# Kernel optimization log

Hardware: AMD Instinct MI355X
Metric: run time of the kernel (lower is better)

## Reference

```python
import jax, jax.numpy as jnp
import numpy as np

LAMBDA = 25.0
MU = 25.0
NU = 1.0
ALPHA = 0.25
EPS = 1e-4
NUM_MATCHES = (20, 4)


def _cdist(a, b):
    # a: (B, Na, D), b: (B, Nb, D) -> euclidean distances (B, Na, Nb)
    d2 = (jnp.sum(a * a, axis=-1)[:, :, None]
          + jnp.sum(b * b, axis=-1)[:, None, :]
          - 2.0 * jnp.einsum('bnd,bmd->bnm', a, b))
    return jnp.sqrt(jnp.maximum(d2, 0.0))


def _nearest_neighbors(input_maps, candidate_maps, distances, num_matches):
    # Faithful to lightly.models.utils.nearest_neighbors:
    #  1) for each input element find its nearest candidate (argmin over last dim)
    #  2) keep the num_matches input elements with smallest nn distance
    # Indices are non-differentiable in torch, so stop_gradient on distances.
    distances = jax.lax.stop_gradient(distances)
    nn_idx = jnp.argmin(distances, axis=-1)           # (B, Na)
    nn_val = jnp.min(distances, axis=-1)              # (B, Na)
    _, min_idx = jax.lax.top_k(-nn_val, num_matches)  # smallest num_matches -> (B, M)
    filt_in = jnp.take_along_axis(input_maps, min_idx[..., None], axis=1)      # (B, M, C)
    cand_nn = jnp.take_along_axis(candidate_maps, nn_idx[..., None], axis=1)   # (B, Na, C)
    filt_cand = jnp.take_along_axis(cand_nn, min_idx[..., None], axis=1)       # (B, M, C)
    return filt_in, filt_cand


def _mse(a, b):
    return jnp.mean((a - b) ** 2)


def _variance_loss(x):
    # torch.var default is unbiased (ddof=1)
    std = jnp.sqrt(jnp.var(x, axis=0, ddof=1) + EPS)
    return jnp.mean(jax.nn.relu(1.0 - std))


def _covariance_loss(x):
    n, d = x.shape
    x = x - jnp.mean(x, axis=0)
    cov = (x.T @ x) / (n - 1)                         # (D, D)
    off = cov - jnp.diag(jnp.diag(cov))
    return jnp.sum(off ** 2) / d


def _global_loss(z_a, z_b):
    inv = _mse(z_a, z_b)
    var = 0.5 * (_variance_loss(z_a) + _variance_loss(z_b))
    cov = _covariance_loss(z_a) + _covariance_loss(z_b)
    return LAMBDA * inv + MU * var + NU * cov


def _local_loss(za, zb, ga, gb):
    B = za.shape[0]
    za = za.reshape(B, -1, za.shape[-1])              # (B, H*W, C)
    zb = zb.reshape(B, -1, zb.shape[-1])
    ga = ga.reshape(B, -1, 2)                          # (B, H*W, 2)
    gb = gb.reshape(B, -1, 2)
    has_local_view = za.shape[1] != zb.shape[1]
    nm = NUM_MATCHES[1] if has_local_view else NUM_MATCHES[0]
    # L2 feature-space matching
    fa, na = _nearest_neighbors(za, zb, _cdist(za, zb), nm)
    fb, nb = _nearest_neighbors(zb, za, _cdist(zb, za), nm)
    inv = 0.5 * _mse(fa, na) + 0.5 * _mse(fb, nb)
    # Grid (spatial) matching
    fa, na = _nearest_neighbors(za, zb, _cdist(ga, gb), NUM_MATCHES[0])
    fb, nb = _nearest_neighbors(zb, za, _cdist(gb, ga), NUM_MATCHES[1])
    inv = inv + 0.5 * _mse(fa, na) + 0.5 * _mse(fb, nb)
    return LAMBDA * inv


def setup_inputs() -> dict:
    key = jax.random.key(0)
    k1, k2, k3, k4, k5, k6 = jax.random.split(key, 6)
    B, D = 128, 8192
    H = W = 7
    return {
        'z_a': jax.random.normal(k1, (B, D), dtype=jnp.float32),
        'z_b': jax.random.normal(k2, (B, D), dtype=jnp.float32),
        'z_a_local_features': jax.random.normal(k3, (B, H, W, D), dtype=jnp.float32),
        'z_b_local_features': jax.random.normal(k4, (B, H, W, D), dtype=jnp.float32),
        'grid_a': jax.random.uniform(k5, (B, H, W, 2), dtype=jnp.float32),
        'grid_b': jax.random.uniform(k6, (B, H, W, 2), dtype=jnp.float32),
    }


def reference(z_a, z_b, z_a_local_features, z_b_local_features, grid_a, grid_b):
    g = _global_loss(z_a, z_b)
    l = _local_loss(z_a_local_features, z_b_local_features, grid_a, grid_b)
    return ALPHA * g + (1.0 - ALPHA) * l
```

## Files before the change

kernel.cpp:

```cpp
#include <hip/hip_runtime.h>
#include <math.h>

#define BATCH 128
#define DIM   8192
#define HW    49
#define PAIRS 2401
#define SLOT  2512

#define WS_MSE    0
#define WS_VARA   1
#define WS_VARB   2
#define WS_DIAGA  3
#define WS_DIAGB  4
#define WS_S1     5
#define WS_S2     6
#define WS_S3     7
#define WS_S4     8
#define WS_SK2A   9
#define WS_SK2B   10
#define WS_TICKET 11
#define COLS_OFF    16
#define GRAMA_OFF   32784
#define GRAMB_OFF   49168
#define GK2PART_OFF 65552
#define L1PART_BIG  2162704
#define WS_NEED_FLOATS (L1PART_BIG + 256 * SLOT)
#define L1PART_SMALL 65552

typedef __attribute__((ext_vector_type(8))) short bf16x8;
typedef __attribute__((ext_vector_type(4))) float f32x4;

__device__ __forceinline__ unsigned cvtpk(float lo, float hi) {
    unsigned r;
    asm("v_cvt_pk_bf16_f32 %0, %1, %2" : "=v"(r) : "v"(lo), "v"(hi));
    return r;
}
__device__ __forceinline__ bf16x8 cvt8(f32x4 a, f32x4 b) {
    union { unsigned u[4]; bf16x8 v; } r;
    r.u[0] = cvtpk(a.x, a.y); r.u[1] = cvtpk(a.z, a.w);
    r.u[2] = cvtpk(b.x, b.y); r.u[3] = cvtpk(b.z, b.w);
    return r.v;
}
__device__ __forceinline__ f32x4 ld4(const unsigned char* p) {
    return *(const f32x4*)p;
}
__device__ __forceinline__ void gload16(const float* g, unsigned char* l) {
    __builtin_amdgcn_global_load_lds(
        (const __attribute__((address_space(1))) void*)g,
        (__attribute__((address_space(3))) void*)l, 16, 0, 0);
}

template<bool RED>
__global__ __launch_bounds__(512) void uber(const float* __restrict__ za_l,
                                            const float* __restrict__ zb_l,
                                            const float* __restrict__ z_a,
                                            const float* __restrict__ z_b,
                                            float* __restrict__ ws,
                                            float* __restrict__ l1part)
{
    __shared__ __align__(16) unsigned char shm[150528];
    const int tid = threadIdx.x;

    if (blockIdx.x < 64) {
        const int chunk = blockIdx.x;
        float* sxA = (float*)shm;
        float* sxB = sxA + 128 * 68;
        float* scr = sxB + 128 * 68;
        const int ty = tid >> 5, tx = tid & 31;
        const int q = tid >> 6, cc = tid & 63;

        float accA[8][4], accB[8][4];
#pragma unroll
        for (int r = 0; r < 8; ++r)
#pragma unroll
            for (int c = 0; c < 4; ++c) { accA[r][c] = 0.f; accB[r][c] = 0.f; }
        float cSA[2] = {0.f,0.f}, cQA[2] = {0.f,0.f};
        float cSB[2] = {0.f,0.f}, cQB[2] = {0.f,0.f};
        float mse = 0.f;

#pragma unroll
        for (int st = 0; st < 2; ++st) {
            __syncthreads();
            for (int f = tid; f < 2048; f += 512) {
                int row = f >> 4, c4 = f & 15;
                const float4 a4 = *(const float4*)(z_a + (size_t)row * DIM + chunk * 128 + st * 64 + c4 * 4);
                const float4 b4 = *(const float4*)(z_b + (size_t)row * DIM + chunk * 128 + st * 64 + c4 * 4);
                *(float4*)(sxA + row * 68 + c4 * 4) = a4;
                *(float4*)(sxB + row * 68 + c4 * 4) = b4;
                float dx = a4.x - b4.x, dy = a4.y - b4.y, dz = a4.z - b4.z, dw = a4.w - b4.w;
                mse += dx * dx + dy * dy + dz * dz + dw * dw;
            }
            __syncthreads();
            for (int r = 0; r < 16; ++r) {
                float vA = sxA[(q * 16 + r) * 68 + cc];
                float vB = sxB[(q * 16 + r) * 68 + cc];
                cSA[st] += vA; cQA[st] += vA * vA;
                cSB[st] += vB; cQB[st] += vB * vB;
            }
            for (int k = 0; k < 64; k += 4) {
                float4 ar4[8], br4[8];
#pragma unroll
                for (int r = 0; r < 8; ++r) {
                    ar4[r] = *(const float4*)(sxA + (ty + 16 * r) * 68 + k);
                    br4[r] = *(const float4*)(sxB + (ty + 16 * r) * 68 + k);
                }
#pragma unroll
                for (int c = 0; c < 4; ++c) {
                    float4 ac4 = *(const float4*)(sxA + (tx + 32 * c) * 68 + k);
                    float4 bc4 = *(const float4*)(sxB + (tx + 32 * c) * 68 + k);
#pragma unroll
                    for (int r = 0; r < 8; ++r) {
                        accA[r][c] += ar4[r].x * ac4.x + ar4[r].y * ac4.y + ar4[r].z * ac4.z + ar4[r].w * ac4.w;
                        accB[r][c] += br4[r].x * bc4.x + br4[r].y * bc4.y + br4[r].z * bc4.z + br4[r].w * bc4.w;
                    }
                }
            }
        }
#pragma unroll
        for (int tens = 0; tens < 2; ++tens) {
            __syncthreads();
            scr[q * 64 + cc]        = tens ? cSB[0] : cSA[0];
            scr[512 + q * 64 + cc]  = tens ? cSB[1] : cSA[1];
            scr[1024 + q * 64 + cc] = tens ? cQB[0] : cQA[0];
            scr[1536 + q * 64 + cc] = tens ? cQB[1] : cQA[1];
            __syncthreads();
            if (tid < 128) {
                int st = tid >> 6, c2 = tid & 63;
                float s = 0.f, qq = 0.f;
#pragma unroll
                for (int g = 0; g < 8; ++g) {
                    s  += scr[st * 512 + g * 64 + c2];
                    qq += scr[1024 + st * 512 + g * 64 + c2];
                }
                int col = chunk * 128 + st * 64 + c2;
                float* C = ws + COLS_OFF + tens * 2 * DIM;
                C[col] = s; C[DIM + col] = qq;
            }
        }
        for (int o = 32; o; o >>= 1) mse += __shfl_xor(mse, o);
        if ((tid & 63) == 0) atomicAdd(&ws[WS_MSE], mse);
        if (RED) {
            float* P = ws + GK2PART_OFF + (size_t)chunk * 32768;
#pragma unroll
            for (int r = 0; r < 8; ++r)
#pragma unroll
                for (int c = 0; c < 4; ++c) {
                    P[(ty + 16 * r) * 128 + tx + 32 * c] = accA[r][c];
                    P[16384 + (ty + 16 * r) * 128 + tx + 32 * c] = accB[r][c];
                }
        } else {
#pragma unroll
            for (int r = 0; r < 8; ++r)
#pragma unroll
                for (int c = 0; c < 4; ++c) {
                    atomicAdd(&ws[GRAMA_OFF + (ty + 16 * r) * 128 + tx + 32 * c], accA[r][c]);
                    atomicAdd(&ws[GRAMB_OFF + (ty + 16 * r) * 128 + tx + 32 * c], accB[r][c]);
                }
        }
        __syncthreads();
    }

    {
        const int lb = blockIdx.x;
        unsigned char* buf0 = shm;
        unsigned char* buf1 = shm + 50176;
        unsigned char* buf2 = shm + 100352;
        const int wv = tid >> 6, lane = tid & 63;
        const int fr = lane & 15, kg = lane >> 4;
        const int batch = lb >> 1;
        const int kh    = lb & 1;
        const float* Az = za_l + (size_t)batch * HW * DIM + (size_t)kh * 4096;
        const float* Bz = zb_l + (size_t)batch * HW * DIM + (size_t)kh * 4096;

        const float* gp[7];
        int jb[7];
        const int half = lane >> 5, l5 = lane & 31;
#pragma unroll
        for (int i = 0; i < 7; ++i) {
            int j = wv + 8 * i;
            gp[i] = Az; jb[i] = -1;
            if (j < 49) {
                int row = 2 * j + half;
                const float* rbase = (row < 49) ? (Az + (size_t)row * DIM)
                                                : (Bz + (size_t)(row - 49) * DIM);
                gp[i] = rbase + ((l5 ^ (row & 31)) << 2);
                jb[i] = j << 10;
            }
        }

        const int wr = wv >> 2, wc = wv & 3;
        int ar0 = wr * 32 + fr;
        int ar1 = ar0 + 16; if (ar1 > 48) ar1 = 48;
        int bc  = wc * 16 + fr; if (bc > 48) bc = 48;
        const int brow = 49 + bc;
        const int aw0 = ar0 << 9, pa0 = ar0 & 31;
        const int aw1 = ar1 << 9, pa1 = ar1 & 31;
        const int bw  = brow << 9, pb = brow & 31;

        f32x4 acc00 = {0.f,0.f,0.f,0.f}, acc10 = {0.f,0.f,0.f,0.f};
        f32x4 aa0 = {0.f,0.f,0.f,0.f}, aa1 = {0.f,0.f,0.f,0.f}, bb = {0.f,0.f,0.f,0.f};

        asm volatile("s_waitcnt vmcnt(0)" ::: "memory");
        __builtin_amdgcn_sched_barrier(0);

#define L1_ISSUE(DST, s) do {                                                  \
    _Pragma("unroll") for (int i = 0; i < 7; ++i)                              \
        if (jb[i] >= 0) gload16(gp[i] + (size_t)(s) * 128, (DST) + jb[i]);     \
    } while (0)

        L1_ISSUE(buf0, 0);
        L1_ISSUE(buf1, 1);

        int m = 0;
#pragma unroll 1
        for (int s = 0; s < 32; ++s) {
            if (s == 31)      asm volatile("s_waitcnt vmcnt(0)" ::: "memory");
            else if (wv == 0) asm volatile("s_waitcnt vmcnt(7)" ::: "memory");
            else              asm volatile("s_waitcnt vmcnt(6)" ::: "memory");
            __builtin_amdgcn_sched_barrier(0);
            __builtin_amdgcn_s_barrier();
            __builtin_amdgcn_sched_barrier(0);
            if (s <= 29) {
                int m2 = m + 2; if (m2 >= 3) m2 -= 3;
                unsigned char* nxt = (m2 == 0) ? buf0 : (m2 == 1) ? buf1 : buf2;
                L1_ISSUE(nxt, s + 2);
                __builtin_amdgcn_sched_barrier(0);
            }
            unsigned char* cur = (m == 0) ? buf0 : (m == 1) ? buf1 : buf2;
#pragma unroll
            for (int kk = 0; kk < 4; ++kk) {
                const int s0 = kk * 8 + kg * 2;
                bf16x8 a0 = cvt8(ld4(cur + aw0 + (((s0)     ^ pa0) << 4)),
                                 ld4(cur + aw0 + (((s0 + 1) ^ pa0) << 4)));
                bf16x8 a1 = cvt8(ld4(cur + aw1 + (((s0)     ^ pa1) << 4)),
                                 ld4(cur + aw1 + (((s0 + 1) ^ pa1) << 4)));
                bf16x8 b0 = cvt8(ld4(cur + bw  + (((s0)     ^ pb ) << 4)),
                                 ld4(cur + bw  + (((s0 + 1) ^ pb ) << 4)));
                acc00 = __builtin_amdgcn_mfma_f32_16x16x32_bf16(a0, b0, acc00, 0, 0, 0);
                acc10 = __builtin_amdgcn_mfma_f32_16x16x32_bf16(a1, b0, acc10, 0, 0, 0);
                aa0   = __builtin_amdgcn_mfma_f32_16x16x32_bf16(a0, a0, aa0,   0, 0, 0);
                aa1   = __builtin_amdgcn_mfma_f32_16x16x32_bf16(a1, a1, aa1,   0, 0, 0);
                bb    = __builtin_amdgcn_mfma_f32_16x16x32_bf16(b0, b0, bb,    0, 0, 0);
            }
            m = (m == 2) ? 0 : m + 1;
        }
#undef L1_ISSUE

        float* gout = l1part + (size_t)(RED ? lb : batch) * SLOT;
        const int gc = wc * 16 + fr;
#pragma unroll
        for (int rr = 0; rr < 4; ++rr) {
            int gr0 = wr * 32 + kg * 4 + rr;
            int gr1 = gr0 + 16;
            if (gc < HW) {
                if (gr0 < HW) {
                    if (RED) gout[gr0 * HW + gc] = acc00[rr];
                    else atomicAdd(&gout[gr0 * HW + gc], acc00[rr]);
                }
                if (gr1 < HW) {
                    if (RED) gout[gr1 * HW + gc] = acc10[rr];
                    else atomicAdd(&gout[gr1 * HW + gc], acc10[rr]);
                }
            }
        }
        if (wc == 0) {
#pragma unroll
            for (int rr = 0; rr < 4; ++rr) {
                int i = kg * 4 + rr;
                if (i == fr) {
                    int r0 = wr * 32 + i;
                    if (RED) gout[PAIRS + r0] = aa0[rr];
                    else atomicAdd(&gout[PAIRS + r0], aa0[rr]);
                    int r1 = r0 + 16;
                    if (r1 < HW) {
                        if (RED) gout[PAIRS + r1] = aa1[rr];
                        else atomicAdd(&gout[PAIRS + r1], aa1[rr]);
                    }
                }
            }
        }
        if (wr == 0) {
#pragma unroll
            for (int rr = 0; rr < 4; ++rr) {
                int i = kg * 4 + rr;
                if (i == fr) {
                    int rb_ = wc * 16 + i;
                    if (rb_ < HW) {
                        if (RED) gout[PAIRS + HW + rb_] = bb[rr];
                        else atomicAdd(&gout[PAIRS + HW + rb_], bb[rr]);
                    }
                }
            }
        }
    }
}

template<bool RED>
__global__ __launch_bounds__(256) void merge2(const float* __restrict__ ga,
                                              const float* __restrict__ gb,
                                              float* __restrict__ ws,
                                              const float* __restrict__ l1part)
{
    __shared__ float d2f[PAIRS];
    __shared__ float d2g[PAIRS];
    __shared__ float nAs[49], nBs[49];
    __shared__ float gax[49], gay[49], gbx[49], gby[49];
    __shared__ float mval[4][49];
    __shared__ int   midx[4][49];

    const int b = blockIdx.x;
    const int tid = threadIdx.x;

    if (b < 128) {
        if (!RED) return;
        int gid = b * 256 + tid;
        int tensor = gid >> 14, e = gid & 16383;
        const float* P = ws + GK2PART_OFF + (size_t)tensor * 16384;
        float s = 0.f;
        for (int c = 0; c < 64; ++c) s += P[(size_t)c * 32768 + e];
        ws[(tensor ? GRAMB_OFF : GRAMA_OFF) + e] = s;
        return;
    }
    if (b < 160) {
        int col = (b - 128) * 256 + tid;
        float sa = ws[COLS_OFF + col];
        float qa = ws[COLS_OFF + DIM + col];
        float sb = ws[COLS_OFF + 2 * DIM + col];
        float qb = ws[COLS_OFF + 3 * DIM + col];
        float sA = qa - sa * sa * (1.0f / BATCH);
        float sB = qb - sb * sb * (1.0f / BATCH);
        float rA = fmaxf(0.f, 1.f - sqrtf(sA * (1.0f / (BATCH - 1)) + 1e-4f));
        float rB = fmaxf(0.f, 1.f - sqrtf(sB * (1.0f / (BATCH - 1)) + 1e-4f));
        float dA = sA * sA, dB = sB * sB;
        for (int o = 32; o; o >>= 1) {
            rA += __shfl_xor(rA, o);
            rB += __shfl_xor(rB, o);
            dA += __shfl_xor(dA, o);
            dB += __shfl_xor(dB, o);
        }
        if ((tid & 63) == 0) {
            atomicAdd(&ws[WS_VARA],  rA);
            atomicAdd(&ws[WS_VARB],  rB);
            atomicAdd(&ws[WS_DIAGA], dA);
            atomicAdd(&ws[WS_DIAGB], dB);
        }
        return;
    }

    const int batch = b - 160;
    const float* P0 = l1part + (size_t)batch * (RED ? (2 * SLOT) : SLOT);
    auto rd = [&](int off) -> float {
        if (!RED) return P0[off];
        return P0[off] + P0[SLOT + off];
    };

    if (tid < 49) nAs[tid] = rd(PAIRS + tid);
    else if (tid >= 64 && tid < 113) nBs[tid - 64] = rd(PAIRS + 49 + (tid - 64));
    if (tid >= 128 && tid < 177) {
        int i = tid - 128;
        gax[i] = ga[batch * 98 + i * 2];
        gay[i] = ga[batch * 98 + i * 2 + 1];
    } else if (tid >= 192 && tid < 241) {
        int i = tid - 192;
        gbx[i] = gb[batch * 98 + i * 2];
        gby[i] = gb[batch * 98 + i * 2 + 1];
    }
    __syncthreads();
    for (int e = tid; e < PAIRS; e += 256) {
        int i = e / 49, j = e - i * 49;
        d2f[e] = nAs[i] + nBs[j] - 2.0f * rd(e);
        float dx = gax[i] - gbx[j], dy = gay[i] - gby[j];
        d2g[e] = dx * dx + dy * dy;
    }
    __syncthreads();
    const int task = tid >> 6, l = tid & 63;
    if (l < 49) {
        float bv = 3.0e38f; int bi = 0;
        if (task == 0) {
            for (int j = 0; j < 49; ++j) { float v = d2f[l * 49 + j]; if (v < bv) { bv = v; bi = j; } }
        } else if (task == 1) {
            for (int i = 0; i < 49; ++i) { float v = d2f[i * 49 + l]; if (v < bv) { bv = v; bi = i; } }
        } else if (task == 2) {
            for (int j = 0; j < 49; ++j) { float v = d2g[l * 49 + j]; if (v < bv) { bv = v; bi = j; } }
        } else {
            for (int i = 0; i < 49; ++i) { float v = d2g[i * 49 + l]; if (v < bv) { bv = v; bi = i; } }
        }
        mval[task][l] = bv; midx[task][l] = bi;
    }
    __syncthreads();
    if (l < 49) {
        float v = mval[task][l];
        int rank = 0;
        for (int k = 0; k < 49; ++k) {
            float u = mval[task][k];
            rank += (u < v) || (u == v && k < l);
        }
        if (task == 0)      { if (rank < 20) atomicAdd(&ws[WS_S1], v); }
        else if (task == 1) { if (rank < 20) atomicAdd(&ws[WS_S2], v); }
        else if (task == 2) { if (rank < 20) atomicAdd(&ws[WS_S3], d2f[l * 49 + midx[2][l]]); }
        else                { if (rank < 4)  atomicAdd(&ws[WS_S4], d2f[midx[3][l] * 49 + l]); }
    }
}

__global__ __launch_bounds__(256) void gk3_final(float* __restrict__ ws,
                                                 float* __restrict__ out)
{
    __shared__ float r[128];
    __shared__ float sS;
    __shared__ float wrd[4];
    const int tid = threadIdx.x;
    const float* G = ws + (blockIdx.x ? GRAMB_OFF : GRAMA_OFF);
    if (tid < 128) {
        float s0 = 0.f, s1 = 0.f, s2 = 0.f, s3 = 0.f;
        for (int k = 0; k < 128; k += 4) {
            s0 += G[(k + 0) * 128 + tid];
            s1 += G[(k + 1) * 128 + tid];
            s2 += G[(k + 2) * 128 + tid];
            s3 += G[(k + 3) * 128 + tid];
        }
        r[tid] = (s0 + s1) + (s2 + s3);
    }
    __syncthreads();
    if (tid < 64) {
        float t = r[tid] + r[tid + 64];
        for (int o = 32; o; o >>= 1) t += __shfl_xor(t, o);
        if (tid == 0) sS = t;
    }
    __syncthreads();
    const float S = sS;
    float sk = 0.f;
    for (int e = tid; e < 16384; e += 256) {
        float K = G[e] - (r[e >> 7] + r[e & 127]) * (1.0f / 128.0f) + S * (1.0f / 16384.0f);
        sk += K * K;
    }
    for (int o = 32; o; o >>= 1) sk += __shfl_xor(sk, o);
    if ((tid & 63) == 0) wrd[tid >> 6] = sk;
    __syncthreads();
    if (tid == 0) {
        ws[blockIdx.x ? WS_SK2B : WS_SK2A] = wrd[0] + wrd[1] + wrd[2] + wrd[3];
        __threadfence();
        unsigned t = atomicAdd((unsigned*)&ws[WS_TICKET], 1u);
        if (t == 1) {
            __threadfence();
            float inv_g = ws[WS_MSE] * (1.0f / ((float)BATCH * (float)DIM));
            float varl  = 0.5f * (ws[WS_VARA] + ws[WS_VARB]) * (1.0f / (float)DIM);
            float cov   = (ws[WS_SK2A] - ws[WS_DIAGA] + ws[WS_SK2B] - ws[WS_DIAGB])
                          * (1.0f / (127.0f * 127.0f * (float)DIM));
            float gl = 25.0f * inv_g + 25.0f * varl + cov;
            float m20 = (float)BATCH * 20.0f * (float)DIM;
            float m4  = (float)BATCH * 4.0f  * (float)DIM;
            float invl = 0.5f * (ws[WS_S1] + ws[WS_S2] + ws[WS_S3]) / m20
                       + 0.5f * ws[WS_S4] / m4;
            out[0] = 0.25f * gl + 0.75f * (25.0f * invl);
        }
    }
}

extern "C" void kernel_launch(void* const* d_in, const int* in_sizes, int n_in,
                              void* d_out, int out_size, void* d_ws, size_t ws_size,
                              hipStream_t stream)
{
    (void)in_sizes; (void)n_in; (void)out_size;
    const float* z_a = (const float*)d_in[0];
    const float* z_b = (const float*)d_in[1];
    const float* zla = (const float*)d_in[2];
    const float* zlb = (const float*)d_in[3];
    const float* ga  = (const float*)d_in[4];
    const float* gb  = (const float*)d_in[5];
    float* ws  = (float*)d_ws;
    float* out = (float*)d_out;

    const bool big = ws_size >= (size_t)WS_NEED_FLOATS * sizeof(float);

    if (big) {
        hipMemsetAsync(d_ws, 0, 16 * sizeof(float), stream);
        uber<true><<<256, 512, 0, stream>>>(zla, zlb, z_a, z_b, ws, ws + L1PART_BIG);
        merge2<true><<<288, 256, 0, stream>>>(ga, gb, ws, ws + L1PART_BIG);
        gk3_final<<<2, 256, 0, stream>>>(ws, out);
    } else {
        hipMemsetAsync(d_ws, 0, (size_t)(L1PART_SMALL + BATCH * SLOT) * sizeof(float), stream);
        uber<false><<<256, 512, 0, stream>>>(zla, zlb, z_a, z_b, ws, ws + L1PART_SMALL);
        merge2<false><<<288, 256, 0, stream>>>(ga, gb, ws, ws + L1PART_SMALL);
        gk3_final<<<2, 256, 0, stream>>>(ws, out);
    }
}
```

Baseline: 131.0 us.

## Stage local-feature tiles through registers as bf16 with double-buffered LDS

Replaces the direct global-to-LDS fp32 copies and triple buffering with register-staged global loads. Each element is converted to bf16 once and written into a half-size, XOR-swizzled LDS buffer, with two buffers alternating. This removes the repeated fp32 to bf16 conversions and doubled LDS reads in the MFMA loop, and halves shared memory so more blocks may fit per CU. In exchange it uses more VGPRs to hold the in-flight loads and adds an extra LDS write and lgkmcnt wait before each barrier.

```diff
diff --git a/kernel.cpp b/kernel.cpp
--- a/kernel.cpp
+++ b/kernel.cpp
@@ -35,20 +35,8 @@
     asm("v_cvt_pk_bf16_f32 %0, %1, %2" : "=v"(r) : "v"(lo), "v"(hi));
     return r;
 }
-__device__ __forceinline__ bf16x8 cvt8(f32x4 a, f32x4 b) {
-    union { unsigned u[4]; bf16x8 v; } r;
-    r.u[0] = cvtpk(a.x, a.y); r.u[1] = cvtpk(a.z, a.w);
-    r.u[2] = cvtpk(b.x, b.y); r.u[3] = cvtpk(b.z, b.w);
-    return r.v;
-}
-__device__ __forceinline__ f32x4 ld4(const unsigned char* p) {
-    return *(const f32x4*)p;
-}
-__device__ __forceinline__ void gload16(const float* g, unsigned char* l) {
-    __builtin_amdgcn_global_load_lds(
-        (const __attribute__((address_space(1))) void*)g,
-        (__attribute__((address_space(3))) void*)l, 16, 0, 0);
-}
+
+#define SB0() __builtin_amdgcn_sched_barrier(0)
 
 template<bool RED>
 __global__ __launch_bounds__(512) void uber(const float* __restrict__ za_l,
@@ -58,7 +46,7 @@
                                             float* __restrict__ ws,
                                             float* __restrict__ l1part)
 {
-    __shared__ __align__(16) unsigned char shm[150528];
+    __shared__ __align__(16) unsigned char shm[81920];
     const int tid = threadIdx.x;
 
     if (blockIdx.x < 64) {
@@ -163,8 +151,7 @@
     {
         const int lb = blockIdx.x;
         unsigned char* buf0 = shm;
-        unsigned char* buf1 = shm + 50176;
-        unsigned char* buf2 = shm + 100352;
+        unsigned char* buf1 = shm + 25088;
         const int wv = tid >> 6, lane = tid & 63;
         const int fr = lane & 15, kg = lane >> 4;
         const int batch = lb >> 1;
@@ -172,19 +159,19 @@
         const float* Az = za_l + (size_t)batch * HW * DIM + (size_t)kh * 4096;
         const float* Bz = zb_l + (size_t)batch * HW * DIM + (size_t)kh * 4096;
 
+        const int half = lane >> 5, l5 = lane & 31;
         const float* gp[7];
-        int jb[7];
-        const int half = lane >> 5, l5 = lane & 31;
+        int wb[7];
 #pragma unroll
         for (int i = 0; i < 7; ++i) {
             int j = wv + 8 * i;
-            gp[i] = Az; jb[i] = -1;
+            gp[i] = Az; wb[i] = -1;
             if (j < 49) {
                 int row = 2 * j + half;
                 const float* rbase = (row < 49) ? (Az + (size_t)row * DIM)
                                                 : (Bz + (size_t)(row - 49) * DIM);
-                gp[i] = rbase + ((l5 ^ (row & 31)) << 2);
-                jb[i] = j << 10;
+                gp[i] = rbase + l5 * 4;
+                wb[i] = row * 256 + ((((l5 >> 1) ^ (row & 15)) << 4) | ((l5 & 1) << 3));
             }
         }
 
@@ -193,58 +180,81 @@
         int ar1 = ar0 + 16; if (ar1 > 48) ar1 = 48;
         int bc  = wc * 16 + fr; if (bc > 48) bc = 48;
         const int brow = 49 + bc;
-        const int aw0 = ar0 << 9, pa0 = ar0 & 31;
-        const int aw1 = ar1 << 9, pa1 = ar1 & 31;
-        const int bw  = brow << 9, pb = brow & 31;
+        const int aw0 = ar0 << 8, pa0 = ar0 & 15;
+        const int aw1 = ar1 << 8, pa1 = ar1 & 15;
+        const int bw  = brow << 8, pb = brow & 15;
 
         f32x4 acc00 = {0.f,0.f,0.f,0.f}, acc10 = {0.f,0.f,0.f,0.f};
         f32x4 aa0 = {0.f,0.f,0.f,0.f}, aa1 = {0.f,0.f,0.f,0.f}, bb = {0.f,0.f,0.f,0.f};
 
+        f32x4 RS0[7], RS1[7];
+
+#define GLOAD(dst, i, s) do {                                                  \
+        if (wb[i] >= 0) {                                                      \
+            const float* p_ = gp[i] + (size_t)(s) * 128;                       \
+            asm volatile("global_load_dwordx4 %0, %1, off"                     \
+                         : "=v"(dst) : "v"(p_) : "memory");                    \
+        } } while (0)
+
+#define L1_LOADS(RS, s) do {                                                   \
+        GLOAD(RS[0], 0, s); GLOAD(RS[1], 1, s); GLOAD(RS[2], 2, s);            \
+        GLOAD(RS[3], 3, s); GLOAD(RS[4], 4, s); GLOAD(RS[5], 5, s);            \
+        GLOAD(RS[6], 6, s); } while (0)
+
+#define L1_CVTWRITE(RS, B) do {                                                \
+        _Pragma("unroll") for (int i = 0; i < 7; ++i)                          \
+            if (wb[i] >= 0) {                                                  \
+                f32x4 v_ = RS[i];                                              \
+                *(uint2*)((B) + wb[i]) =                                       \
+                    make_uint2(cvtpk(v_.x, v_.y), cvtpk(v_.z, v_.w));          \
+            } } while (0)
+
+#define L1_COMPUTE(B) do {                                                     \
+        _Pragma("unroll") for (int kk = 0; kk < 4; ++kk) {                     \
+            const int s0_ = kk * 4 + kg;                                       \
+            bf16x8 a0 = *(const bf16x8*)((B) + aw0 + (((s0_) ^ pa0) << 4));    \
+            bf16x8 a1 = *(const bf16x8*)((B) + aw1 + (((s0_) ^ pa1) << 4));    \
+            bf16x8 b0 = *(const bf16x8*)((B) + bw  + (((s0_) ^ pb ) << 4));    \
+            acc00 = __builtin_amdgcn_mfma_f32_16x16x32_bf16(a0, b0, acc00, 0, 0, 0); \
+            acc10 = __builtin_amdgcn_mfma_f32_16x16x32_bf16(a1, b0, acc10, 0, 0, 0); \
+            aa0   = __builtin_amdgcn_mfma_f32_16x16x32_bf16(a0, a0, aa0,   0, 0, 0); \
+            aa1   = __builtin_amdgcn_mfma_f32_16x16x32_bf16(a1, a1, aa1,   0, 0, 0); \
+            bb    = __builtin_amdgcn_mfma_f32_16x16x32_bf16(b0, b0, bb,    0, 0, 0); \
+        } } while (0)
+
+#define VMWAIT_STEADY() do {                                                   \
+        if (wv == 0) asm volatile("s_waitcnt vmcnt(7)" ::: "memory");          \
+        else         asm volatile("s_waitcnt vmcnt(6)" ::: "memory");          \
+        } while (0)
+
         asm volatile("s_waitcnt vmcnt(0)" ::: "memory");
-        __builtin_amdgcn_sched_barrier(0);
-
-#define L1_ISSUE(DST, s) do {                                                  \
-    _Pragma("unroll") for (int i = 0; i < 7; ++i)                              \
-        if (jb[i] >= 0) gload16(gp[i] + (size_t)(s) * 128, (DST) + jb[i]);     \
-    } while (0)
-
-        L1_ISSUE(buf0, 0);
-        L1_ISSUE(buf1, 1);
-
-        int m = 0;
+        SB0();
+
+        L1_LOADS(RS0, 0); SB0();
+        L1_LOADS(RS1, 1); SB0();
+
 #pragma unroll 1
-        for (int s = 0; s < 32; ++s) {
-            if (s == 31)      asm volatile("s_waitcnt vmcnt(0)" ::: "memory");
-            else if (wv == 0) asm volatile("s_waitcnt vmcnt(7)" ::: "memory");
-            else              asm volatile("s_waitcnt vmcnt(6)" ::: "memory");
-            __builtin_amdgcn_sched_barrier(0);
-            __builtin_amdgcn_s_barrier();
-            __builtin_amdgcn_sched_barrier(0);
-            if (s <= 29) {
-                int m2 = m + 2; if (m2 >= 3) m2 -= 3;
-                unsigned char* nxt = (m2 == 0) ? buf0 : (m2 == 1) ? buf1 : buf2;
-                L1_ISSUE(nxt, s + 2);
-                __builtin_amdgcn_sched_barrier(0);
-            }
-            unsigned char* cur = (m == 0) ? buf0 : (m == 1) ? buf1 : buf2;
-#pragma unroll
-            for (int kk = 0; kk < 4; ++kk) {
-                const int s0 = kk * 8 + kg * 2;
-                bf16x8 a0 = cvt8(ld4(cur + aw0 + (((s0)     ^ pa0) << 4)),
-                                 ld4(cur + aw0 + (((s0 + 1) ^ pa0) << 4)));
-                bf16x8 a1 = cvt8(ld4(cur + aw1 + (((s0)     ^ pa1) << 4)),
-                                 ld4(cur + aw1 + (((s0 + 1) ^ pa1) << 4)));
-                bf16x8 b0 = cvt8(ld4(cur + bw  + (((s0)     ^ pb ) << 4)),
-                                 ld4(cur + bw  + (((s0 + 1) ^ pb ) << 4)));
-                acc00 = __builtin_amdgcn_mfma_f32_16x16x32_bf16(a0, b0, acc00, 0, 0, 0);
-                acc10 = __builtin_amdgcn_mfma_f32_16x16x32_bf16(a1, b0, acc10, 0, 0, 0);
-                aa0   = __builtin_amdgcn_mfma_f32_16x16x32_bf16(a0, a0, aa0,   0, 0, 0);
-                aa1   = __builtin_amdgcn_mfma_f32_16x16x32_bf16(a1, a1, aa1,   0, 0, 0);
-                bb    = __builtin_amdgcn_mfma_f32_16x16x32_bf16(b0, b0, bb,    0, 0, 0);
-            }
-            m = (m == 2) ? 0 : m + 1;
-        }
-#undef L1_ISSUE
+        for (int s = 0; s < 32; s += 2) {
+            VMWAIT_STEADY(); SB0();
+            L1_CVTWRITE(RS0, buf0);
+            asm volatile("s_waitcnt lgkmcnt(0)" ::: "memory"); SB0();
+            __builtin_amdgcn_s_barrier(); SB0();
+            if (s + 2 < 32) { L1_LOADS(RS0, s + 2); SB0(); }
+            L1_COMPUTE(buf0);
+            if (s + 1 == 31) asm volatile("s_waitcnt vmcnt(0)" ::: "memory");
+            else             VMWAIT_STEADY();
+            SB0();
+            L1_CVTWRITE(RS1, buf1);
+            asm volatile("s_waitcnt lgkmcnt(0)" ::: "memory"); SB0();
+            __builtin_amdgcn_s_barrier(); SB0();
+            if (s + 3 < 32) { L1_LOADS(RS1, s + 3); SB0(); }
+            L1_COMPUTE(buf1);
+        }
+#undef GLOAD
+#undef L1_LOADS
+#undef L1_CVTWRITE
+#undef L1_COMPUTE
+#undef VMWAIT_STEADY
 
         float* gout = l1part + (size_t)(RED ? lb : batch) * SLOT;
         const int gc = wc * 16 + fr;
```

New measurement: 121.4 us. 1.08x faster.
